# Performance work log

Hardware: AMD Instinct MI355X
Metric: run time of the kernel (lower is better)

## Reference

```python
import jax, jax.numpy as jnp
import numpy as np

NUM_HEADS = 16
KEY_SIZE = 64
MODEL = NUM_HEADS * KEY_SIZE
B, S = 4, 2048
NEG = jnp.float32(-1e9)


def alibi_bidirectional_bias(num_heads, seq_len):
    # slopes for num_heads//2 heads: 1 / x**(i+1), x = 24**(1/h)
    h = num_heads // 2
    x = 24.0 ** (1.0 / h)
    slopes = (1.0 / x ** jnp.arange(1, h + 1, dtype=jnp.float32))[:, None, None]  # [h,1,1]
    i = jnp.arange(seq_len)
    rel = (i[None, :] - i[:, None]).astype(jnp.float32)  # rel[i,j] = j - i
    # forward (causal): tril(j - i) + (-1e9 strictly above diag)
    fwd = slopes * jnp.tril(rel) + jnp.triu(jnp.full((seq_len, seq_len), NEG), k=1)
    # backward (anti-causal): triu(i - j) + (-1e9 strictly below diag)
    bwd = slopes * jnp.triu(-rel) + jnp.tril(jnp.full((seq_len, seq_len), NEG), k=-1)
    return jnp.concatenate([fwd, bwd], axis=0)  # [num_heads, S, S]


def setup_inputs() -> dict:
    key = jax.random.key(0)
    ks = jax.random.split(key, 11)
    sc = 0.02
    d = {
        "query": jax.random.normal(ks[0], (B, S, MODEL), jnp.float32),
        "key": jax.random.normal(ks[1], (B, S, MODEL), jnp.float32),
        "value": jax.random.normal(ks[2], (B, S, MODEL), jnp.float32),
        "Wq": jax.random.normal(ks[3], (MODEL, MODEL), jnp.float32) * sc,
        "bq": jnp.zeros((MODEL,), jnp.float32),
        "Wk": jax.random.normal(ks[4], (MODEL, MODEL), jnp.float32) * sc,
        "bk": jnp.zeros((MODEL,), jnp.float32),
        "Wv": jax.random.normal(ks[5], (MODEL, MODEL), jnp.float32) * sc,
        "bv": jnp.zeros((MODEL,), jnp.float32),
        "Wo": jax.random.normal(ks[6], (MODEL, MODEL), jnp.float32) * sc,
        "bo": jnp.zeros((MODEL,), jnp.float32),
    }
    return d


def reference(query, key, value, Wq, bq, Wk, bk, Wv, bv, Wo, bo):
    b, s, _ = query.shape
    H, D = NUM_HEADS, KEY_SIZE

    def proj(x, W, bias):
        return (x @ W.T + bias).reshape(b, s, H, D).transpose(0, 2, 1, 3)  # [B,H,S,D]

    q = proj(query, Wq, bq)
    k = proj(key, Wk, bk)
    v = proj(value, Wv, bv)

    bias = alibi_bidirectional_bias(H, s)  # [H,S,S], broadcasts over batch
    scores = jnp.einsum("bhqd,bhkd->bhqk", q, k) / jnp.sqrt(jnp.float32(D)) + bias
    attn = jax.nn.softmax(scores, axis=-1)
    out = jnp.einsum("bhqk,bhkd->bhqd", attn, v)
    out = out.transpose(0, 2, 1, 3).reshape(b, s, H * D)
    return out @ Wo.T + bo
```

## Files before the change

kernel.cpp:

```cpp
#include <hip/hip_runtime.h>
#include <hip/hip_bf16.h>
#include <stdint.h>

typedef unsigned short u16;
typedef __attribute__((ext_vector_type(8))) __bf16 bf16x8;
typedef __attribute__((ext_vector_type(4))) __bf16 bf16x4;
typedef __attribute__((ext_vector_type(4))) float f32x4;

#define S_LEN 2048
#define NHEAD 16
#define HDIM 64
#define DMODEL 1024
#define NBATCH 4
#define MTOK (NBATCH * S_LEN)

__device__ __forceinline__ u16 f2bf(float f) {
    uint32_t u = __float_as_uint(f);
    u += 0x7fffu + ((u >> 16) & 1u);
    return (u16)(u >> 16);
}

__device__ __forceinline__ void gld_lds16(const u16* g, u16* l) {
    __builtin_amdgcn_global_load_lds(
        (const __attribute__((address_space(1))) void*)g,
        (__attribute__((address_space(3))) void*)l, 16, 0, 0);
}

__global__ __launch_bounds__(256) void cast_all(
        const float* __restrict__ q, const float* __restrict__ k, const float* __restrict__ v,
        const float* __restrict__ wq, const float* __restrict__ wk,
        const float* __restrict__ wv, const float* __restrict__ wo,
        u16* __restrict__ xq, u16* __restrict__ xk, u16* __restrict__ xv,
        u16* __restrict__ wqb, u16* __restrict__ wkb, u16* __restrict__ wvb,
        u16* __restrict__ wob) {
    size_t idx4 = (size_t)blockIdx.x * 256 + threadIdx.x;
    const float* src;
    u16* dst;
    size_t off;
    if (idx4 < (size_t)3 << 21) {
        int t = (int)(idx4 >> 21);
        off = (idx4 & ((1u << 21) - 1)) * 4;
        src = (t == 0) ? q : (t == 1) ? k : v;
        dst = (t == 0) ? xq : (t == 1) ? xk : xv;
    } else {
        size_t w = idx4 - ((size_t)3 << 21);
        int t = (int)(w >> 18);
        off = (w & ((1u << 18) - 1)) * 4;
        src = (t == 0) ? wq : (t == 1) ? wk : (t == 2) ? wv : wo;
        dst = (t == 0) ? wqb : (t == 1) ? wkb : (t == 2) ? wvb : wob;
    }
    float4 val = *(const float4*)(src + off);
    ushort4 o;
    o.x = f2bf(val.x); o.y = f2bf(val.y); o.z = f2bf(val.z); o.w = f2bf(val.w);
    *(ushort4*)(dst + off) = o;
}

#define TM 128
#define TN 128
#define BK 64

__device__ __forceinline__ void gemm_body(const u16* __restrict__ A,
                                          const u16* __restrict__ W,
                                          const float* __restrict__ bias,
                                          void* __restrict__ outp, int mode,
                                          int m0, int n0) {
    __shared__ __align__(16) u16 As[2][TM * BK];
    __shared__ __align__(16) u16 Bs[2][TM * BK];
    const int tid  = threadIdx.x;
    const int lane = tid & 63;
    const int wv   = tid >> 6;
    const int l16  = lane & 15;
    const int quad = lane >> 4;
    const int wm   = (wv >> 1) * 64;
    const int wn   = (wv & 1) * 64;

    f32x4 acc[4][4];
#pragma unroll
    for (int i = 0; i < 4; i++)
#pragma unroll
        for (int j = 0; j < 4; j++) acc[i][j] = {};

    const int sr  = lane >> 3;
    const int sc7 = (lane & 7) ^ sr;
    const u16* gA = A + (size_t)(m0 + wv * 32 + sr) * DMODEL + sc7 * 8;
    const u16* gB = W + (size_t)(n0 + wv * 32 + sr) * DMODEL + sc7 * 8;
    const int lofs = wv * 32 * BK;

    const int cA = quad ^ (l16 & 7);
    const int cB = (quad + 4) ^ (l16 & 7);

#pragma unroll
    for (int g = 0; g < 4; g++) {
        gld_lds16(gA + (size_t)(g * 8) * DMODEL, &As[0][lofs + g * 8 * BK]);
        gld_lds16(gB + (size_t)(g * 8) * DMODEL, &Bs[0][lofs + g * 8 * BK]);
    }
    __builtin_amdgcn_s_waitcnt(0x0F70);
    __syncthreads();

    int buf = 0;
    for (int kb = 0; kb < DMODEL; kb += BK) {
        const bool more = (kb + BK < DMODEL);
        if (more) {
#pragma unroll
            for (int g = 0; g < 4; g++) {
                gld_lds16(gA + kb + BK + (size_t)(g * 8) * DMODEL,
                          &As[buf ^ 1][lofs + g * 8 * BK]);
                gld_lds16(gB + kb + BK + (size_t)(g * 8) * DMODEL,
                          &Bs[buf ^ 1][lofs + g * 8 * BK]);
            }
        }
        __builtin_amdgcn_sched_barrier(0);

        bf16x8 af0[4], af1[4], bf0[4], bf1[4];
#pragma unroll
        for (int i = 0; i < 4; i++) {
            const u16* ap = &As[buf][(wm + i * 16 + l16) * BK];
            af0[i] = *(const bf16x8*)(ap + cA * 8);
            af1[i] = *(const bf16x8*)(ap + cB * 8);
        }
#pragma unroll
        for (int j = 0; j < 4; j++) {
            const u16* bp = &Bs[buf][(wn + j * 16 + l16) * BK];
            bf0[j] = *(const bf16x8*)(bp + cA * 8);
            bf1[j] = *(const bf16x8*)(bp + cB * 8);
        }
#pragma unroll
        for (int i = 0; i < 4; i++)
#pragma unroll
            for (int j = 0; j < 4; j++)
                acc[i][j] = __builtin_amdgcn_mfma_f32_16x16x32_bf16(af0[i], bf0[j], acc[i][j], 0, 0, 0);
#pragma unroll
        for (int i = 0; i < 4; i++)
#pragma unroll
            for (int j = 0; j < 4; j++)
                acc[i][j] = __builtin_amdgcn_mfma_f32_16x16x32_bf16(af1[i], bf1[j], acc[i][j], 0, 0, 0);

        if (more) __builtin_amdgcn_s_waitcnt(0x0F70);
        __syncthreads();
        buf ^= 1;
    }

#pragma unroll
    for (int j = 0; j < 4; j++) {
        int n = n0 + wn + j * 16 + l16;
        float bv = bias[n];
#pragma unroll
        for (int i = 0; i < 4; i++) {
            int mbase = m0 + wm + i * 16 + quad * 4;
#pragma unroll
            for (int r = 0; r < 4; r++) {
                int m = mbase + r;
                float v = acc[i][j][r] + bv;
                if (mode == 2) {
                    ((float*)outp)[(size_t)m * DMODEL + n] = v;
                } else {
                    int b = m >> 11, s = m & (S_LEN - 1);
                    int h = n >> 6, d = n & 63;
                    u16* o = (u16*)outp;
                    size_t idx = (mode == 0)
                        ? ((((size_t)(b * NHEAD + h)) * S_LEN + s) * HDIM + d)
                        : ((((size_t)(b * NHEAD + h)) * HDIM + d) * S_LEN + s);
                    o[idx] = f2bf(v);
                }
            }
        }
    }
}

__device__ __forceinline__ void gemm_coords(int& m0, int& n0) {
    const int lid = blockIdx.x + 8 * blockIdx.y;
    const int xcd = lid & 7;
    const int s   = lid >> 3;
    n0 = (s & 7) * TN;
    m0 = ((s >> 3) + 8 * xcd) * TM;
}

__global__ __launch_bounds__(256) void gemm_qkv(
        const u16* __restrict__ xq, const u16* __restrict__ xk, const u16* __restrict__ xv,
        const u16* __restrict__ wq, const u16* __restrict__ wk, const u16* __restrict__ wv,
        const float* __restrict__ bq, const float* __restrict__ bk, const float* __restrict__ bv,
        u16* __restrict__ Qb, u16* __restrict__ Kb, u16* __restrict__ Vb) {
    int z = blockIdx.z;
    const u16* A   = (z == 0) ? xq : (z == 1) ? xk : xv;
    const u16* W   = (z == 0) ? wq : (z == 1) ? wk : wv;
    const float* b = (z == 0) ? bq : (z == 1) ? bk : bv;
    u16* out       = (z == 0) ? Qb : (z == 1) ? Kb : Vb;
    int m0, n0;
    gemm_coords(m0, n0);
    gemm_body(A, W, b, out, (z == 2) ? 1 : 0, m0, n0);
}

__global__ __launch_bounds__(256) void gemm_one(
        const u16* __restrict__ A, const u16* __restrict__ W,
        const float* __restrict__ bias, void* __restrict__ out, int mode) {
    int m0, n0;
    gemm_coords(m0, n0);
    gemm_body(A, W, bias, out, mode, m0, n0);
}

__global__ __launch_bounds__(256, 4) void flash_kernel(
        const u16* __restrict__ Q, const u16* __restrict__ K,
        const u16* __restrict__ Vt, u16* __restrict__ AO) {
    __shared__ __align__(16) u16 Ksm[2][64 * 64];
    __shared__ __align__(16) u16 Vsm[2][64 * 64];
    __shared__ __align__(16) u16 Psm[4][16 * 64];

    const int tid  = threadIdx.x;
    const int wv   = tid >> 6;
    const int lane = tid & 63;
    const int l16  = lane & 15;
    const int quad = lane >> 4;

    const int lid   = blockIdx.x + 16 * blockIdx.y;
    const int xcd   = lid & 7;
    const int slot  = lid >> 3;
    const int bh    = xcd + 8 * (slot >> 4);
    const int g_idx = slot & 15;

    const int h    = bh & (NHEAD - 1);
    const int b    = bh >> 4;
    const bool fwd = (h < 8);
    const int sgn  = fwd ? 1 : -1;
    const float slope2 = __builtin_amdgcn_exp2f(-(float)((h & 7) + 1) * 0.5731203125901445f)
                         * 1.4426950408889634f;
    const float cL = 0.18033688011112042f;

    const u16* Kg = K + (size_t)bh * S_LEN * HDIM;
    const u16* Vg = Vt + (size_t)bh * HDIM * S_LEN;

    const int sr = lane >> 3;
    const int sc = (lane & 7) ^ sr;
    const int r0 = 16 * wv;

    const int cA = quad ^ (l16 & 7);
    const int cB = (quad + 4) ^ (l16 & 7);

    float brt[4][4];
#pragma unroll
    for (int t = 0; t < 4; t++)
#pragma unroll
        for (int r = 0; r < 4; r++)
            brt[t][r] = slope2 * (float)(sgn * (16 * t + 4 * quad + r - l16)) - 16.0f;

    int poff4[4];
#pragma unroll
    for (int t = 0; t < 4; t++)
        poff4[t] = l16 * 64 + (((2 * t + (quad >> 1)) ^ (l16 & 7)) * 8) + 4 * (quad & 1);

    bf16x8 ones;
#pragma unroll
    for (int j = 0; j < 8; j++) ones[j] = (__bf16)1.0f;

    const float dkq = slope2 * (float)(sgn * 64);

#pragma unroll 1
    for (int half = 0; half < 2; half++) {
        const int g  = half ? (31 - g_idx) : g_idx;
        const int q0 = g * 64 + wv * 16;
        const u16* Qp = Q + ((size_t)bh * S_LEN + q0) * HDIM;
        const bf16x8 aq0 = *(const bf16x8*)(Qp + l16 * HDIM + quad * 8);
        const bf16x8 aq1 = *(const bf16x8*)(Qp + l16 * HDIM + 32 + quad * 8);

        f32x4 o[4], osum = {};
#pragma unroll
        for (int dt = 0; dt < 4; dt++) o[dt] = {};

        const int kt0 = fwd ? 0 : g;
        const int kt1 = fwd ? g : (S_LEN / 64 - 1);

        __syncthreads();
        const u16* kg = Kg + ((size_t)(kt0 * 64) + r0 + sr) * 64 + sc * 8;
        const u16* vg = Vg + (size_t)(r0 + sr) * S_LEN + kt0 * 64 + sc * 8;
        gld_lds16(kg,              &Ksm[0][r0 * 64]);
        gld_lds16(kg + 8 * 64,     &Ksm[0][(r0 + 8) * 64]);
        gld_lds16(vg,              &Vsm[0][r0 * 64]);
        gld_lds16(vg + 8 * S_LEN,  &Vsm[0][(r0 + 8) * 64]);
        kg += 64 * 64;
        vg += 64;

        float kq = slope2 * (float)(sgn * (kt0 * 64 - q0));

        int buf = 0;
        for (int kt = kt0; kt <= kt1; ++kt) {
            __builtin_amdgcn_s_waitcnt(0x0F70);
            __syncthreads();
            if (kt < kt1) {
                gld_lds16(kg,             &Ksm[buf ^ 1][r0 * 64]);
                gld_lds16(kg + 8 * 64,    &Ksm[buf ^ 1][(r0 + 8) * 64]);
                gld_lds16(vg,             &Vsm[buf ^ 1][r0 * 64]);
                gld_lds16(vg + 8 * S_LEN, &Vsm[buf ^ 1][(r0 + 8) * 64]);
                kg += 64 * 64;
                vg += 64;
            }
            const u16* Ks = &Ksm[buf][0];
            const u16* Vs = &Vsm[buf][0];

            f32x4 st[4];
#pragma unroll
            for (int t = 0; t < 4; t++) {
                const u16* kp = Ks + (16 * t + l16) * 64;
                bf16x8 k0 = *(const bf16x8*)(kp + cA * 8);
                bf16x8 k1 = *(const bf16x8*)(kp + cB * 8);
                f32x4 c = {};
                c = __builtin_amdgcn_mfma_f32_16x16x32_bf16(k0, aq0, c, 0, 0, 0);
                c = __builtin_amdgcn_mfma_f32_16x16x32_bf16(k1, aq1, c, 0, 0, 0);
                st[t] = c;
            }

            float p[4][4];
            if (kt == g) {
                const int qg = q0 + l16;
#pragma unroll
                for (int t = 0; t < 4; t++)
#pragma unroll
                    for (int r = 0; r < 4; r++) {
                        const int kg2 = kt * 64 + 16 * t + 4 * quad + r;
                        const bool ok = fwd ? (kg2 <= qg) : (kg2 >= qg);
                        float s2 = fmaf(st[t][r], cL, brt[t][r] + kq);
                        p[t][r] = ok ? __builtin_amdgcn_exp2f(s2) : 0.0f;
                    }
            } else {
#pragma unroll
                for (int t = 0; t < 4; t++)
#pragma unroll
                    for (int r = 0; r < 4; r++)
                        p[t][r] = __builtin_amdgcn_exp2f(fmaf(st[t][r], cL, brt[t][r] + kq));
            }
            kq += dkq;

            u16* Pw = &Psm[wv][0];
#pragma unroll
            for (int t = 0; t < 4; t++) {
                bf16x4 pk;
                pk[0] = (__bf16)p[t][0];
                pk[1] = (__bf16)p[t][1];
                pk[2] = (__bf16)p[t][2];
                pk[3] = (__bf16)p[t][3];
                *(bf16x4*)(Pw + poff4[t]) = pk;
            }
            __builtin_amdgcn_s_waitcnt(0xC07F);
            bf16x8 pf0 = *(const bf16x8*)(&Pw[l16 * 64 + cA * 8]);
            bf16x8 pf1 = *(const bf16x8*)(&Pw[l16 * 64 + cB * 8]);

#pragma unroll
            for (int dt = 0; dt < 4; dt++) {
                const u16* vp = Vs + (dt * 16 + l16) * 64;
                bf16x8 v0 = *(const bf16x8*)(vp + cA * 8);
                bf16x8 v1 = *(const bf16x8*)(vp + cB * 8);
                o[dt] = __builtin_amdgcn_mfma_f32_16x16x32_bf16(pf0, v0, o[dt], 0, 0, 0);
                o[dt] = __builtin_amdgcn_mfma_f32_16x16x32_bf16(pf1, v1, o[dt], 0, 0, 0);
            }
            osum = __builtin_amdgcn_mfma_f32_16x16x32_bf16(pf0, ones, osum, 0, 0, 0);
            osum = __builtin_amdgcn_mfma_f32_16x16x32_bf16(pf1, ones, osum, 0, 0, 0);
            buf ^= 1;
        }

#pragma unroll
        for (int r = 0; r < 4; r++) {
            float inv = 1.0f / osum[r];
            int qg = q0 + quad * 4 + r;
            u16* op = AO + ((size_t)b * S_LEN + qg) * DMODEL + h * HDIM;
#pragma unroll
            for (int dt = 0; dt < 4; dt++)
                op[dt * 16 + l16] = f2bf(o[dt][r] * inv);
        }
    }
}

extern "C" void kernel_launch(void* const* d_in, const int* in_sizes, int n_in,
                              void* d_out, int out_size, void* d_ws, size_t ws_size,
                              hipStream_t stream) {
    const float* query = (const float*)d_in[0];
    const float* key   = (const float*)d_in[1];
    const float* value = (const float*)d_in[2];
    const float* Wq    = (const float*)d_in[3];
    const float* bq    = (const float*)d_in[4];
    const float* Wk    = (const float*)d_in[5];
    const float* bk    = (const float*)d_in[6];
    const float* Wv    = (const float*)d_in[7];
    const float* bv    = (const float*)d_in[8];
    const float* Wo    = (const float*)d_in[9];
    const float* bo    = (const float*)d_in[10];

    const size_t Xe = (size_t)MTOK * DMODEL;
    const size_t We = (size_t)DMODEL * DMODEL;
    u16* xq  = (u16*)d_ws;
    u16* xk  = xq + Xe;
    u16* xv  = xk + Xe;
    u16* wqb = xv + Xe;
    u16* wkb = wqb + We;
    u16* wvb = wkb + We;
    u16* wob = wvb + We;
    u16* Qb  = wob + We;
    u16* Kb  = Qb + Xe;
    u16* Vb  = Kb + Xe;
    u16* AO  = Vb + Xe;

    cast_all<<<dim3(28672), dim3(256), 0, stream>>>(
        query, key, value, Wq, Wk, Wv, Wo,
        xq, xk, xv, wqb, wkb, wvb, wob);

    gemm_qkv<<<dim3(DMODEL / TN, MTOK / TM, 3), dim3(256), 0, stream>>>(
        xq, xk, xv, wqb, wkb, wvb, bq, bk, bv, Qb, Kb, Vb);

    flash_kernel<<<dim3(16, NBATCH * NHEAD), dim3(256), 0, stream>>>(Qb, Kb, Vb, AO);

    gemm_one<<<dim3(DMODEL / TN, MTOK / TM, 1), dim3(256), 0, stream>>>(AO, wob, bo, d_out, 2);
}
```

Baseline: 309.7 us.

## Fuse fp32-to-bf16 casts into GEMM tile loads, drop separate cast kernel

Removes the standalone cast kernel and has the projection GEMMs read fp32 activations and weights directly. Each tile is converted to bf16 in registers and written into LDS. This avoids a full write and re-read of bf16 copies of the inputs and weights, plus one launch. In exchange the GEMMs lose async global-to-LDS loads for converted operands, hold fp32 staging registers across the MFMA loop, read twice the bytes per tile, and re-convert weights in every block.

```diff
diff --git a/kernel.cpp b/kernel.cpp
--- a/kernel.cpp
+++ b/kernel.cpp
@@ -26,41 +26,20 @@
         (__attribute__((address_space(3))) void*)l, 16, 0, 0);
 }
 
-__global__ __launch_bounds__(256) void cast_all(
-        const float* __restrict__ q, const float* __restrict__ k, const float* __restrict__ v,
-        const float* __restrict__ wq, const float* __restrict__ wk,
-        const float* __restrict__ wv, const float* __restrict__ wo,
-        u16* __restrict__ xq, u16* __restrict__ xk, u16* __restrict__ xv,
-        u16* __restrict__ wqb, u16* __restrict__ wkb, u16* __restrict__ wvb,
-        u16* __restrict__ wob) {
-    size_t idx4 = (size_t)blockIdx.x * 256 + threadIdx.x;
-    const float* src;
-    u16* dst;
-    size_t off;
-    if (idx4 < (size_t)3 << 21) {
-        int t = (int)(idx4 >> 21);
-        off = (idx4 & ((1u << 21) - 1)) * 4;
-        src = (t == 0) ? q : (t == 1) ? k : v;
-        dst = (t == 0) ? xq : (t == 1) ? xk : xv;
-    } else {
-        size_t w = idx4 - ((size_t)3 << 21);
-        int t = (int)(w >> 18);
-        off = (w & ((1u << 18) - 1)) * 4;
-        src = (t == 0) ? wq : (t == 1) ? wk : (t == 2) ? wv : wo;
-        dst = (t == 0) ? wqb : (t == 1) ? wkb : (t == 2) ? wvb : wob;
-    }
-    float4 val = *(const float4*)(src + off);
-    ushort4 o;
-    o.x = f2bf(val.x); o.y = f2bf(val.y); o.z = f2bf(val.z); o.w = f2bf(val.w);
-    *(ushort4*)(dst + off) = o;
+__device__ __forceinline__ bf16x8 cvt8(float4 lo, float4 hi) {
+    bf16x8 r;
+    r[0] = (__bf16)lo.x; r[1] = (__bf16)lo.y; r[2] = (__bf16)lo.z; r[3] = (__bf16)lo.w;
+    r[4] = (__bf16)hi.x; r[5] = (__bf16)hi.y; r[6] = (__bf16)hi.z; r[7] = (__bf16)hi.w;
+    return r;
 }
 
 #define TM 128
 #define TN 128
 #define BK 64
 
-__device__ __forceinline__ void gemm_body(const u16* __restrict__ A,
-                                          const u16* __restrict__ W,
+template <bool AF32>
+__device__ __forceinline__ void gemm_body(const void* __restrict__ Ap,
+                                          const float* __restrict__ Wf,
                                           const float* __restrict__ bias,
                                           void* __restrict__ outp, int mode,
                                           int m0, int n0) {
@@ -82,31 +61,57 @@
 
     const int sr  = lane >> 3;
     const int sc7 = (lane & 7) ^ sr;
-    const u16* gA = A + (size_t)(m0 + wv * 32 + sr) * DMODEL + sc7 * 8;
-    const u16* gB = W + (size_t)(n0 + wv * 32 + sr) * DMODEL + sc7 * 8;
+    const u16*   gA16 = (const u16*)Ap  + (size_t)(m0 + wv * 32 + sr) * DMODEL + sc7 * 8;
+    const float* gA32 = (const float*)Ap + (size_t)(m0 + wv * 32 + sr) * DMODEL + sc7 * 8;
+    const float* gB32 = Wf + (size_t)(n0 + wv * 32 + sr) * DMODEL + sc7 * 8;
     const int lofs = wv * 32 * BK;
 
     const int cA = quad ^ (l16 & 7);
     const int cB = (quad + 4) ^ (l16 & 7);
 
-#pragma unroll
-    for (int g = 0; g < 4; g++) {
-        gld_lds16(gA + (size_t)(g * 8) * DMODEL, &As[0][lofs + g * 8 * BK]);
-        gld_lds16(gB + (size_t)(g * 8) * DMODEL, &Bs[0][lofs + g * 8 * BK]);
+    {
+        float4 fA[4][2], fB[4][2];
+#pragma unroll
+        for (int g = 0; g < 4; g++) {
+            const float* pb = gB32 + (size_t)(g * 8) * DMODEL;
+            fB[g][0] = *(const float4*)pb;
+            fB[g][1] = *(const float4*)(pb + 4);
+            if constexpr (AF32) {
+                const float* pa = gA32 + (size_t)(g * 8) * DMODEL;
+                fA[g][0] = *(const float4*)pa;
+                fA[g][1] = *(const float4*)(pa + 4);
+            } else {
+                gld_lds16(gA16 + (size_t)(g * 8) * DMODEL, &As[0][lofs + g * 8 * BK]);
+            }
+        }
+        __builtin_amdgcn_s_waitcnt(0x0F70);
+#pragma unroll
+        for (int g = 0; g < 4; g++) {
+            *(bf16x8*)(&Bs[0][lofs + g * 8 * BK + lane * 8]) = cvt8(fB[g][0], fB[g][1]);
+            if constexpr (AF32)
+                *(bf16x8*)(&As[0][lofs + g * 8 * BK + lane * 8]) = cvt8(fA[g][0], fA[g][1]);
+        }
+        __syncthreads();
     }
-    __builtin_amdgcn_s_waitcnt(0x0F70);
-    __syncthreads();
 
     int buf = 0;
     for (int kb = 0; kb < DMODEL; kb += BK) {
         const bool more = (kb + BK < DMODEL);
+        float4 fA[4][2], fB[4][2];
         if (more) {
 #pragma unroll
             for (int g = 0; g < 4; g++) {
-                gld_lds16(gA + kb + BK + (size_t)(g * 8) * DMODEL,
-                          &As[buf ^ 1][lofs + g * 8 * BK]);
-                gld_lds16(gB + kb + BK + (size_t)(g * 8) * DMODEL,
-                          &Bs[buf ^ 1][lofs + g * 8 * BK]);
+                const float* pb = gB32 + kb + BK + (size_t)(g * 8) * DMODEL;
+                fB[g][0] = *(const float4*)pb;
+                fB[g][1] = *(const float4*)(pb + 4);
+                if constexpr (AF32) {
+                    const float* pa = gA32 + kb + BK + (size_t)(g * 8) * DMODEL;
+                    fA[g][0] = *(const float4*)pa;
+                    fA[g][1] = *(const float4*)(pa + 4);
+                } else {
+                    gld_lds16(gA16 + kb + BK + (size_t)(g * 8) * DMODEL,
+                              &As[buf ^ 1][lofs + g * 8 * BK]);
+                }
             }
         }
         __builtin_amdgcn_sched_barrier(0);
@@ -135,7 +140,15 @@
             for (int j = 0; j < 4; j++)
                 acc[i][j] = __builtin_amdgcn_mfma_f32_16x16x32_bf16(af1[i], bf1[j], acc[i][j], 0, 0, 0);
 
-        if (more) __builtin_amdgcn_s_waitcnt(0x0F70);
+        if (more) {
+            __builtin_amdgcn_s_waitcnt(0x0F70);
+#pragma unroll
+            for (int g = 0; g < 4; g++) {
+                *(bf16x8*)(&Bs[buf ^ 1][lofs + g * 8 * BK + lane * 8]) = cvt8(fB[g][0], fB[g][1]);
+                if constexpr (AF32)
+                    *(bf16x8*)(&As[buf ^ 1][lofs + g * 8 * BK + lane * 8]) = cvt8(fA[g][0], fA[g][1]);
+            }
+        }
         __syncthreads();
         buf ^= 1;
     }
@@ -175,27 +188,27 @@
     m0 = ((s >> 3) + 8 * xcd) * TM;
 }
 
-__global__ __launch_bounds__(256) void gemm_qkv(
-        const u16* __restrict__ xq, const u16* __restrict__ xk, const u16* __restrict__ xv,
-        const u16* __restrict__ wq, const u16* __restrict__ wk, const u16* __restrict__ wv,
+__global__ __launch_bounds__(256, 2) void gemm_qkv(
+        const float* __restrict__ q, const float* __restrict__ k, const float* __restrict__ v,
+        const float* __restrict__ wq, const float* __restrict__ wk, const float* __restrict__ wvp,
         const float* __restrict__ bq, const float* __restrict__ bk, const float* __restrict__ bv,
         u16* __restrict__ Qb, u16* __restrict__ Kb, u16* __restrict__ Vb) {
     int z = blockIdx.z;
-    const u16* A   = (z == 0) ? xq : (z == 1) ? xk : xv;
-    const u16* W   = (z == 0) ? wq : (z == 1) ? wk : wv;
+    const float* A = (z == 0) ? q : (z == 1) ? k : v;
+    const float* W = (z == 0) ? wq : (z == 1) ? wk : wvp;
     const float* b = (z == 0) ? bq : (z == 1) ? bk : bv;
     u16* out       = (z == 0) ? Qb : (z == 1) ? Kb : Vb;
     int m0, n0;
     gemm_coords(m0, n0);
-    gemm_body(A, W, b, out, (z == 2) ? 1 : 0, m0, n0);
-}
-
-__global__ __launch_bounds__(256) void gemm_one(
-        const u16* __restrict__ A, const u16* __restrict__ W,
+    gemm_body<true>(A, W, b, out, (z == 2) ? 1 : 0, m0, n0);
+}
+
+__global__ __launch_bounds__(256, 2) void gemm_one(
+        const u16* __restrict__ A, const float* __restrict__ W,
         const float* __restrict__ bias, void* __restrict__ out, int mode) {
     int m0, n0;
     gemm_coords(m0, n0);
-    gemm_body(A, W, bias, out, mode, m0, n0);
+    gemm_body<false>(A, W, bias, out, mode, m0, n0);
 }
 
 __global__ __launch_bounds__(256, 4) void flash_kernel(
@@ -383,27 +396,15 @@
     const float* bo    = (const float*)d_in[10];
 
     const size_t Xe = (size_t)MTOK * DMODEL;
-    const size_t We = (size_t)DMODEL * DMODEL;
-    u16* xq  = (u16*)d_ws;
-    u16* xk  = xq + Xe;
-    u16* xv  = xk + Xe;
-    u16* wqb = xv + Xe;
-    u16* wkb = wqb + We;
-    u16* wvb = wkb + We;
-    u16* wob = wvb + We;
-    u16* Qb  = wob + We;
-    u16* Kb  = Qb + Xe;
-    u16* Vb  = Kb + Xe;
-    u16* AO  = Vb + Xe;
-
-    cast_all<<<dim3(28672), dim3(256), 0, stream>>>(
-        query, key, value, Wq, Wk, Wv, Wo,
-        xq, xk, xv, wqb, wkb, wvb, wob);
+    u16* Qb = (u16*)d_ws;
+    u16* Kb = Qb + Xe;
+    u16* Vb = Kb + Xe;
+    u16* AO = Vb + Xe;
 
     gemm_qkv<<<dim3(DMODEL / TN, MTOK / TM, 3), dim3(256), 0, stream>>>(
-        xq, xk, xv, wqb, wkb, wvb, bq, bk, bv, Qb, Kb, Vb);
+        query, key, value, Wq, Wk, Wv, bq, bk, bv, Qb, Kb, Vb);
 
     flash_kernel<<<dim3(16, NBATCH * NHEAD), dim3(256), 0, stream>>>(Qb, Kb, Vb, AO);
 
-    gemm_one<<<dim3(DMODEL / TN, MTOK / TM, 1), dim3(256), 0, stream>>>(AO, wob, bo, d_out, 2);
-}
+    gemm_one<<<dim3(DMODEL / TN, MTOK / TM, 1), dim3(256), 0, stream>>>(AO, Wo, bo, d_out, 2);
+}
```

New measurement: 379.0 us. 22.4% more time.

## Fuse both query halves into one K/V pass to share tile loads

Applied to the files above, without the earlier changes.

The flash kernel used to process its two query groups (g and 31-g) in sequence, each streaming its own range of K/V tiles. Now one loop covers the union of the two ranges, and each K/V tile loaded into shared memory is applied to both query groups. This halves redundant K/V global loads and barriers, and also adds s_setprio hints around the MFMA sections and computes the bias terms incrementally. The costs are more registers for two sets of accumulators, which may lower occupancy, and reuse of the xq workspace buffer for the attention output.

```diff
diff --git a/kernel.cpp b/kernel.cpp
--- a/kernel.cpp
+++ b/kernel.cpp
@@ -235,12 +235,12 @@
     const int cA = quad ^ (l16 & 7);
     const int cB = (quad + 4) ^ (l16 & 7);
 
-    float brt[4][4];
-#pragma unroll
-    for (int t = 0; t < 4; t++)
-#pragma unroll
-        for (int r = 0; r < 4; r++)
-            brt[t][r] = slope2 * (float)(sgn * (16 * t + 4 * quad + r - l16)) - 16.0f;
+    float base_r[4];
+#pragma unroll
+    for (int r = 0; r < 4; r++)
+        base_r[r] = slope2 * (float)(sgn * (4 * quad + r - l16)) - 16.0f;
+    const float dt16 = slope2 * (float)(sgn * 16);
+    const float dkq  = slope2 * (float)(sgn * 64);
 
     int poff4[4];
 #pragma unroll
@@ -251,118 +251,126 @@
 #pragma unroll
     for (int j = 0; j < 8; j++) ones[j] = (__bf16)1.0f;
 
-    const float dkq = slope2 * (float)(sgn * 64);
-
+    const int g0 = g_idx, g1 = 31 - g_idx;
+    const int q00 = g0 * 64 + wv * 16;
+    const int q01 = g1 * 64 + wv * 16;
+    const int ktA = fwd ? 0 : g0;
+    const int ktB = fwd ? g1 : 31;
+
+    const u16* Qp0 = Q + ((size_t)bh * S_LEN + q00) * HDIM;
+    const u16* Qp1 = Q + ((size_t)bh * S_LEN + q01) * HDIM;
+    const bf16x8 aq00 = *(const bf16x8*)(Qp0 + l16 * HDIM + quad * 8);
+    const bf16x8 aq01 = *(const bf16x8*)(Qp0 + l16 * HDIM + 32 + quad * 8);
+    const bf16x8 aq10 = *(const bf16x8*)(Qp1 + l16 * HDIM + quad * 8);
+    const bf16x8 aq11 = *(const bf16x8*)(Qp1 + l16 * HDIM + 32 + quad * 8);
+
+    f32x4 o0[4], o1[4], osum0 = {}, osum1 = {};
+#pragma unroll
+    for (int dt = 0; dt < 4; dt++) { o0[dt] = {}; o1[dt] = {}; }
+
+    float kq0 = slope2 * (float)(sgn * (ktA * 64 - q00));
+    float kq1 = slope2 * (float)(sgn * (ktA * 64 - q01));
+
+    const u16* kg = Kg + ((size_t)(ktA * 64) + r0 + sr) * 64 + sc * 8;
+    const u16* vg = Vg + (size_t)(r0 + sr) * S_LEN + ktA * 64 + sc * 8;
+    gld_lds16(kg,              &Ksm[0][r0 * 64]);
+    gld_lds16(kg + 8 * 64,     &Ksm[0][(r0 + 8) * 64]);
+    gld_lds16(vg,              &Vsm[0][r0 * 64]);
+    gld_lds16(vg + 8 * S_LEN,  &Vsm[0][(r0 + 8) * 64]);
+    kg += 64 * 64;
+    vg += 64;
+
+#define DO_HALF(aqA, aqB, oo, os, kqv, gh, q0h) do {                          \
+    if (fwd ? (kt <= (gh)) : (kt >= (gh))) {                                  \
+        f32x4 st[4];                                                          \
+        __builtin_amdgcn_s_setprio(1);                                        \
+        _Pragma("unroll")                                                     \
+        for (int t = 0; t < 4; t++) {                                         \
+            const u16* kp = Ks + (16 * t + l16) * 64;                         \
+            bf16x8 k0 = *(const bf16x8*)(kp + cA * 8);                        \
+            bf16x8 k1 = *(const bf16x8*)(kp + cB * 8);                        \
+            f32x4 c = {};                                                     \
+            c = __builtin_amdgcn_mfma_f32_16x16x32_bf16(k0, aqA, c, 0, 0, 0); \
+            c = __builtin_amdgcn_mfma_f32_16x16x32_bf16(k1, aqB, c, 0, 0, 0); \
+            st[t] = c;                                                        \
+        }                                                                     \
+        __builtin_amdgcn_s_setprio(0);                                        \
+        const bool diag = (kt == (gh));                                       \
+        const int qg = (q0h) + l16;                                           \
+        _Pragma("unroll")                                                     \
+        for (int t = 0; t < 4; t++) {                                         \
+            const float kb2 = (kqv) + (float)t * dt16;                        \
+            bf16x4 pk;                                                        \
+            _Pragma("unroll")                                                 \
+            for (int r = 0; r < 4; r++) {                                     \
+                float s2 = fmaf(st[t][r], cL, base_r[r] + kb2);               \
+                float pv = __builtin_amdgcn_exp2f(s2);                        \
+                if (diag) {                                                   \
+                    const int kk = kt * 64 + 16 * t + 4 * quad + r;           \
+                    const bool ok = fwd ? (kk <= qg) : (kk >= qg);            \
+                    pv = ok ? pv : 0.0f;                                      \
+                }                                                             \
+                pk[r] = (__bf16)pv;                                           \
+            }                                                                 \
+            *(bf16x4*)(Pw + poff4[t]) = pk;                                   \
+        }                                                                     \
+        __builtin_amdgcn_s_waitcnt(0xC07F);                   \
+        bf16x8 pf0 = *(const bf16x8*)(&Pw[l16 * 64 + cA * 8]);                \
+        bf16x8 pf1 = *(const bf16x8*)(&Pw[l16 * 64 + cB * 8]);                \
+        __builtin_amdgcn_s_waitcnt(0xC07F);                                   \
+        __builtin_amdgcn_s_setprio(1);                                        \
+        _Pragma("unroll")                                                     \
+        for (int dt = 0; dt < 4; dt++) {                                      \
+            const u16* vp = Vs + (dt * 16 + l16) * 64;                        \
+            bf16x8 v0 = *(const bf16x8*)(vp + cA * 8);                        \
+            bf16x8 v1 = *(const bf16x8*)(vp + cB * 8);                        \
+            oo[dt] = __builtin_amdgcn_mfma_f32_16x16x32_bf16(pf0, v0, oo[dt], 0, 0, 0); \
+            oo[dt] = __builtin_amdgcn_mfma_f32_16x16x32_bf16(pf1, v1, oo[dt], 0, 0, 0); \
+        }                                                                     \
+        os = __builtin_amdgcn_mfma_f32_16x16x32_bf16(pf0, ones, os, 0, 0, 0); \
+        os = __builtin_amdgcn_mfma_f32_16x16x32_bf16(pf1, ones, os, 0, 0, 0); \
+        __builtin_amdgcn_s_setprio(0);                                        \
+    }                                                                         \
+} while (0)
+
+    int buf = 0;
 #pragma unroll 1
-    for (int half = 0; half < 2; half++) {
-        const int g  = half ? (31 - g_idx) : g_idx;
-        const int q0 = g * 64 + wv * 16;
-        const u16* Qp = Q + ((size_t)bh * S_LEN + q0) * HDIM;
-        const bf16x8 aq0 = *(const bf16x8*)(Qp + l16 * HDIM + quad * 8);
-        const bf16x8 aq1 = *(const bf16x8*)(Qp + l16 * HDIM + 32 + quad * 8);
-
-        f32x4 o[4], osum = {};
-#pragma unroll
-        for (int dt = 0; dt < 4; dt++) o[dt] = {};
-
-        const int kt0 = fwd ? 0 : g;
-        const int kt1 = fwd ? g : (S_LEN / 64 - 1);
-
+    for (int kt = ktA; kt <= ktB; ++kt) {
+        __builtin_amdgcn_s_waitcnt(0x0F70);
         __syncthreads();
-        const u16* kg = Kg + ((size_t)(kt0 * 64) + r0 + sr) * 64 + sc * 8;
-        const u16* vg = Vg + (size_t)(r0 + sr) * S_LEN + kt0 * 64 + sc * 8;
-        gld_lds16(kg,              &Ksm[0][r0 * 64]);
-        gld_lds16(kg + 8 * 64,     &Ksm[0][(r0 + 8) * 64]);
-        gld_lds16(vg,              &Vsm[0][r0 * 64]);
-        gld_lds16(vg + 8 * S_LEN,  &Vsm[0][(r0 + 8) * 64]);
-        kg += 64 * 64;
-        vg += 64;
-
-        float kq = slope2 * (float)(sgn * (kt0 * 64 - q0));
-
-        int buf = 0;
-        for (int kt = kt0; kt <= kt1; ++kt) {
-            __builtin_amdgcn_s_waitcnt(0x0F70);
-            __syncthreads();
-            if (kt < kt1) {
-                gld_lds16(kg,             &Ksm[buf ^ 1][r0 * 64]);
-                gld_lds16(kg + 8 * 64,    &Ksm[buf ^ 1][(r0 + 8) * 64]);
-                gld_lds16(vg,             &Vsm[buf ^ 1][r0 * 64]);
-                gld_lds16(vg + 8 * S_LEN, &Vsm[buf ^ 1][(r0 + 8) * 64]);
-                kg += 64 * 64;
-                vg += 64;
-            }
-            const u16* Ks = &Ksm[buf][0];
-            const u16* Vs = &Vsm[buf][0];
-
-            f32x4 st[4];
-#pragma unroll
-            for (int t = 0; t < 4; t++) {
-                const u16* kp = Ks + (16 * t + l16) * 64;
-                bf16x8 k0 = *(const bf16x8*)(kp + cA * 8);
-                bf16x8 k1 = *(const bf16x8*)(kp + cB * 8);
-                f32x4 c = {};
-                c = __builtin_amdgcn_mfma_f32_16x16x32_bf16(k0, aq0, c, 0, 0, 0);
-                c = __builtin_amdgcn_mfma_f32_16x16x32_bf16(k1, aq1, c, 0, 0, 0);
-                st[t] = c;
-            }
-
-            float p[4][4];
-            if (kt == g) {
-                const int qg = q0 + l16;
-#pragma unroll
-                for (int t = 0; t < 4; t++)
-#pragma unroll
-                    for (int r = 0; r < 4; r++) {
-                        const int kg2 = kt * 64 + 16 * t + 4 * quad + r;
-                        const bool ok = fwd ? (kg2 <= qg) : (kg2 >= qg);
-                        float s2 = fmaf(st[t][r], cL, brt[t][r] + kq);
-                        p[t][r] = ok ? __builtin_amdgcn_exp2f(s2) : 0.0f;
-                    }
-            } else {
-#pragma unroll
-                for (int t = 0; t < 4; t++)
-#pragma unroll
-                    for (int r = 0; r < 4; r++)
-                        p[t][r] = __builtin_amdgcn_exp2f(fmaf(st[t][r], cL, brt[t][r] + kq));
-            }
-            kq += dkq;
-
-            u16* Pw = &Psm[wv][0];
-#pragma unroll
-            for (int t = 0; t < 4; t++) {
-                bf16x4 pk;
-                pk[0] = (__bf16)p[t][0];
-                pk[1] = (__bf16)p[t][1];
-                pk[2] = (__bf16)p[t][2];
-                pk[3] = (__bf16)p[t][3];
-                *(bf16x4*)(Pw + poff4[t]) = pk;
-            }
-            __builtin_amdgcn_s_waitcnt(0xC07F);
-            bf16x8 pf0 = *(const bf16x8*)(&Pw[l16 * 64 + cA * 8]);
-            bf16x8 pf1 = *(const bf16x8*)(&Pw[l16 * 64 + cB * 8]);
-
-#pragma unroll
-            for (int dt = 0; dt < 4; dt++) {
-                const u16* vp = Vs + (dt * 16 + l16) * 64;
-                bf16x8 v0 = *(const bf16x8*)(vp + cA * 8);
-                bf16x8 v1 = *(const bf16x8*)(vp + cB * 8);
-                o[dt] = __builtin_amdgcn_mfma_f32_16x16x32_bf16(pf0, v0, o[dt], 0, 0, 0);
-                o[dt] = __builtin_amdgcn_mfma_f32_16x16x32_bf16(pf1, v1, o[dt], 0, 0, 0);
-            }
-            osum = __builtin_amdgcn_mfma_f32_16x16x32_bf16(pf0, ones, osum, 0, 0, 0);
-            osum = __builtin_amdgcn_mfma_f32_16x16x32_bf16(pf1, ones, osum, 0, 0, 0);
-            buf ^= 1;
-        }
-
-#pragma unroll
-        for (int r = 0; r < 4; r++) {
-            float inv = 1.0f / osum[r];
-            int qg = q0 + quad * 4 + r;
-            u16* op = AO + ((size_t)b * S_LEN + qg) * DMODEL + h * HDIM;
-#pragma unroll
-            for (int dt = 0; dt < 4; dt++)
-                op[dt * 16 + l16] = f2bf(o[dt][r] * inv);
+        if (kt < ktB) {
+            gld_lds16(kg,             &Ksm[buf ^ 1][r0 * 64]);
+            gld_lds16(kg + 8 * 64,    &Ksm[buf ^ 1][(r0 + 8) * 64]);
+            gld_lds16(vg,             &Vsm[buf ^ 1][r0 * 64]);
+            gld_lds16(vg + 8 * S_LEN, &Vsm[buf ^ 1][(r0 + 8) * 64]);
+            kg += 64 * 64;
+            vg += 64;
+        }
+        const u16* Ks = &Ksm[buf][0];
+        const u16* Vs = &Vsm[buf][0];
+        u16* Pw = &Psm[wv][0];
+
+        DO_HALF(aq00, aq01, o0, osum0, kq0, g0, q00);
+        DO_HALF(aq10, aq11, o1, osum1, kq1, g1, q01);
+
+        kq0 += dkq;
+        kq1 += dkq;
+        buf ^= 1;
+    }
+#undef DO_HALF
+
+#pragma unroll
+    for (int r = 0; r < 4; r++) {
+        float inv0 = 1.0f / osum0[r];
+        float inv1 = 1.0f / osum1[r];
+        int qg0 = q00 + quad * 4 + r;
+        int qg1 = q01 + quad * 4 + r;
+        u16* op0 = AO + ((size_t)b * S_LEN + qg0) * DMODEL + h * HDIM;
+        u16* op1 = AO + ((size_t)b * S_LEN + qg1) * DMODEL + h * HDIM;
+#pragma unroll
+        for (int dt = 0; dt < 4; dt++) {
+            op0[dt * 16 + l16] = f2bf(o0[dt][r] * inv0);
+            op1[dt * 16 + l16] = f2bf(o1[dt][r] * inv1);
         }
     }
 }
@@ -394,7 +402,7 @@
     u16* Qb  = wob + We;
     u16* Kb  = Qb + Xe;
     u16* Vb  = Kb + Xe;
-    u16* AO  = Vb + Xe;
+    u16* AO  = xq;
 
     cast_all<<<dim3(28672), dim3(256), 0, stream>>>(
         query, key, value, Wq, Wk, Wv, Wo,
@@ -405,5 +413,5 @@
 
     flash_kernel<<<dim3(16, NBATCH * NHEAD), dim3(256), 0, stream>>>(Qb, Kb, Vb, AO);
 
-    gemm_one<<<dim3(DMODEL / TN, MTOK / TM, 1), dim3(256), 0, stream>>>(AO, wob, bo, d_out, 2);
-}
+    gemm_one<<<dim3(DMODEL / TN, MTOK / TM), dim3(256), 0, stream>>>(AO, wob, bo, d_out, 2);
+}
```

New measurement: 312.5 us. About the same (+0.9%).
